# Optimization experiments

Hardware: AMD Instinct MI355X
Metric: run time of the kernel (lower is better)

The kernel has to match this reference:

```python
import jax, jax.numpy as jnp
import numpy as np

N, D, B, C, T, TOD = 8192, 32, 2, 8, 12, 288
PARAM_SCALE = 0.3  # keep relu+softmax logits well-conditioned (original uses plain randn init)


def setup_inputs() -> dict:
    key = jax.random.key(0)
    k0, k1, k2, k3, k4 = jax.random.split(key, 5)
    return {
        "x": jax.random.normal(k0, (B, C, N, T), dtype=jnp.float32),
        "nodevec1": PARAM_SCALE * jax.random.normal(k1, (N, D), dtype=jnp.float32),
        "nodevec2": PARAM_SCALE * jax.random.normal(k2, (N, D), dtype=jnp.float32),
        "timevec": PARAM_SCALE * jax.random.normal(k3, (TOD, D), dtype=jnp.float32),
        "k": PARAM_SCALE * jax.random.normal(k4, (D, D, D), dtype=jnp.float32),
        "time_ind": 100,
    }


def reference(x, nodevec1, nodevec2, timevec, k, time_ind):
    # Dynamic Tucker-decomposition adjacency (SpatialGraphConv.forward, eval mode -> dropout is identity)
    tv = timevec[time_ind]                             # [D]   time_vec
    core = jnp.einsum('d,def->ef', tv, k)              # [D,D] adp1 (squeezed)
    # adp2/adp3 chain: (nodevec1 @ core) @ nodevec2.T  -> [N,N]
    adp = jnp.einsum('ne,ef->nf', nodevec1, core)      # [N,D]
    adp = jnp.einsum('nf,mf->nm', adp, nodevec2)       # [N,N]
    adp = jax.nn.softmax(jax.nn.relu(adp), axis=-1)    # row-softmax over neighbors
    # NConv: neighbor aggregation  'bcnt,nm->bcmt'
    return jnp.einsum('bcnt,nm->bcmt', x, adp)
```

## Files before the change

kernel.cpp:

```cpp
#include <hip/hip_runtime.h>
#include <hip/hip_bf16.h>


#define NN 8192
#define DD 32
#define TT 12
#define NSPLIT 8
#define CHUNK 1024
#define ESTR 72

typedef __attribute__((ext_vector_type(8))) short bf16x8;
typedef __attribute__((ext_vector_type(4))) short bf16x4;
typedef __attribute__((ext_vector_type(4))) float f32x4;

static __device__ __forceinline__ unsigned short f2bf(float f) {
  unsigned int u = __float_as_uint(f);
  u = (u + 0x7FFFu + ((u >> 16) & 1u)) >> 16;
  return (unsigned short)u;
}

__global__ __launch_bounds__(256) void k_prep(const float* __restrict__ nv1,
                                              const float* __restrict__ nv2,
                                              const float* __restrict__ timevec,
                                              const float* __restrict__ kk,
                                              const int* __restrict__ tind,
                                              unsigned short* __restrict__ t1b,
                                              unsigned short* __restrict__ nv2b) {
  __shared__ float cs[1024];
  const int tid = threadIdx.x;
  const float* tv = timevec + (size_t)tind[0] * DD;
  for (int idx = tid; idx < 1024; idx += 256) {
    float acc = 0.f;
#pragma unroll
    for (int d = 0; d < DD; ++d) acc += tv[d] * kk[d * 1024 + idx];
    cs[idx] = acc;
  }
  __syncthreads();
  const int nbase = blockIdx.x * 128;
  const int f = tid & 31, sub = tid >> 5;
#pragma unroll 4
  for (int it = 0; it < 16; ++it) {
    const int n = nbase + it * 8 + sub;
    const float* nr = nv1 + (size_t)n * DD;
    float acc = 0.f;
#pragma unroll
    for (int e = 0; e < DD; ++e) acc += nr[e] * cs[e * DD + f];
    t1b[(size_t)n * DD + f] = f2bf(acc);
  }
#pragma unroll 4
  for (int it = 0; it < 16; ++it) {
    const int idx = nbase * DD + it * 256 + tid;
    nv2b[idx] = f2bf(nv2[idx]);
  }
}

__global__ __launch_bounds__(256) void k_stats(const unsigned short* __restrict__ t1b,
                                               const unsigned short* __restrict__ nv2b,
                                               float* __restrict__ sums) {
  const int tid = threadIdx.x;
  const int w = tid >> 6, lane = tid & 63, q = lane >> 4, i16 = lane & 15;
  const int nbase = blockIdx.x * 64 + w * 16;
  bf16x8 a = *(const bf16x8*)(t1b + (size_t)(nbase + i16) * DD + q * 8);
  const f32x4 z4 = {0.f, 0.f, 0.f, 0.f};
  float s[4] = {0.f, 0.f, 0.f, 0.f};
  const int m0 = blockIdx.y * 2048;
  for (int mt = m0; mt < m0 + 2048; mt += 64) {
#pragma unroll
    for (int u = 0; u < 4; ++u) {
      bf16x8 b = *(const bf16x8*)(nv2b + (size_t)(mt + u * 16 + i16) * DD + q * 8);
      f32x4 d = __builtin_amdgcn_mfma_f32_16x16x32_bf16(a, b, z4, 0, 0, 0);
#pragma unroll
      for (int r = 0; r < 4; ++r) s[r] += __expf(fmaxf(d[r], 0.f));
    }
  }
#pragma unroll
  for (int r = 0; r < 4; ++r)
    for (int off = 1; off < 16; off <<= 1) s[r] += __shfl_xor(s[r], off, 64);
  if (i16 == 0) {
#pragma unroll
    for (int r = 0; r < 4; ++r) atomicAdd(&sums[nbase + q * 4 + r], s[r]);
  }
}

__global__ __launch_bounds__(256) void k_y(const float* __restrict__ x,
                                           const float* __restrict__ sums,
                                           unsigned short* __restrict__ yT) {
  __shared__ float xs[3072];
  const int tid = threadIdx.x;
  const int n0 = blockIdx.x * 256;
  const int bc = blockIdx.y;
  const float* xp = x + (size_t)bc * NN * TT + (size_t)n0 * TT;
#pragma unroll
  for (int j = 0; j < 12; ++j) xs[j * 256 + tid] = xp[j * 256 + tid];
  __syncthreads();
  const float rinv = 1.0f / sums[n0 + tid];
#pragma unroll
  for (int t = 0; t < 12; ++t)
    yT[(size_t)(bc * TT + t) * NN + n0 + tid] = f2bf(xs[tid * 12 + t] * rinv);
}

__global__ __launch_bounds__(256, 2) void k_mega(const unsigned short* __restrict__ t1b,
                                                 const unsigned short* __restrict__ nv2b,
                                                 const unsigned short* __restrict__ yT,
                                                 float* __restrict__ part) {
  const int tid = threadIdx.x;
  const int w = tid >> 6, lane = tid & 63, q = lane >> 4, i16 = lane & 15;
  const int wc = w & 1, wm = w >> 1;
  const int mb = blockIdx.x * 128;
  const int nt0 = blockIdx.y * CHUNK;

  __shared__ unsigned short Ew[2][128][ESTR];

  bf16x8 bg[2];
#pragma unroll
  for (int g = 0; g < 2; ++g)
    bg[g] = *(const bf16x8*)(nv2b + (size_t)(mb + w * 32 + g * 16 + i16) * DD + q * 8);

  const f32x4 z4 = {0.f, 0.f, 0.f, 0.f};
  f32x4 acc[6][4];
#pragma unroll
  for (int c = 0; c < 6; ++c)
#pragma unroll
    for (int ms = 0; ms < 4; ++ms) acc[c][ms] = (f32x4){0.f, 0.f, 0.f, 0.f};

  {
    bf16x8 atL[4];
#pragma unroll
    for (int s = 0; s < 4; ++s)
      atL[s] = *(const bf16x8*)(t1b + (size_t)(nt0 + s * 16 + i16) * DD + q * 8);
#pragma unroll
    for (int g = 0; g < 2; ++g)
#pragma unroll
      for (int s = 0; s < 4; ++s) {
        f32x4 d = __builtin_amdgcn_mfma_f32_16x16x32_bf16(atL[s], bg[g], z4, 0, 0, 0);
        bf16x4 e;
#pragma unroll
        for (int r = 0; r < 4; ++r) e[r] = (short)f2bf(__expf(fmaxf(d[r], 0.f)));
        *(bf16x4*)&Ew[0][w * 32 + g * 16 + i16][s * 16 + q * 4] = e;
      }
  }
  __syncthreads();

  int p = 0;
  for (int st = 0; st < 16; ++st, p ^= 1) {
    const int nt = nt0 + st * 64;
    const bool more = (st < 15);

    bf16x8 atn[4];
    if (more) {
#pragma unroll
      for (int s = 0; s < 4; ++s)
        atn[s] = *(const bf16x8*)(t1b + (size_t)(nt + 64 + s * 16 + i16) * DD + q * 8);
    }

    bf16x8 yfr0[6];
#pragma unroll
    for (int c = 0; c < 6; ++c)
      yfr0[c] = *(const bf16x8*)(yT + (size_t)((wc * 6 + c) * 16 + i16) * NN + nt + q * 8);
    bf16x8 efr0[4];
#pragma unroll
    for (int ms = 0; ms < 4; ++ms)
      efr0[ms] = *(const bf16x8*)&Ew[p][wm * 64 + ms * 16 + i16][q * 8];

    f32x4 d[2][4];
    if (more) {
#pragma unroll
      for (int g = 0; g < 2; ++g)
#pragma unroll
        for (int s = 0; s < 4; ++s)
          d[g][s] = __builtin_amdgcn_mfma_f32_16x16x32_bf16(atn[s], bg[g], z4, 0, 0, 0);
    }

    bf16x8 yfr1[6];
#pragma unroll
    for (int c = 0; c < 6; ++c)
      yfr1[c] = *(const bf16x8*)(yT + (size_t)((wc * 6 + c) * 16 + i16) * NN + nt + 32 + q * 8);
    bf16x8 efr1[4];
#pragma unroll
    for (int ms = 0; ms < 4; ++ms)
      efr1[ms] = *(const bf16x8*)&Ew[p][wm * 64 + ms * 16 + i16][32 + q * 8];

#pragma unroll
    for (int c = 0; c < 6; ++c)
#pragma unroll
      for (int ms = 0; ms < 4; ++ms)
        acc[c][ms] = __builtin_amdgcn_mfma_f32_16x16x32_bf16(yfr0[c], efr0[ms], acc[c][ms], 0, 0, 0);

    if (more) {
#pragma unroll
      for (int g = 0; g < 2; ++g)
#pragma unroll
        for (int s = 0; s < 4; ++s) {
          bf16x4 e;
#pragma unroll
          for (int r = 0; r < 4; ++r) e[r] = (short)f2bf(__expf(fmaxf(d[g][s][r], 0.f)));
          *(bf16x4*)&Ew[p ^ 1][w * 32 + g * 16 + i16][s * 16 + q * 4] = e;
        }
    }

#pragma unroll
    for (int c = 0; c < 6; ++c)
#pragma unroll
      for (int ms = 0; ms < 4; ++ms)
        acc[c][ms] = __builtin_amdgcn_mfma_f32_16x16x32_bf16(yfr1[c], efr1[ms], acc[c][ms], 0, 0, 0);

    __syncthreads();
  }

  float* pp = part + (size_t)blockIdx.y * 192 * NN;
#pragma unroll
  for (int c = 0; c < 6; ++c)
#pragma unroll
    for (int ms = 0; ms < 4; ++ms) {
      const int colbase = (wc * 6 + c) * 16 + q * 4;
      const int m = mb + wm * 64 + ms * 16 + i16;
#pragma unroll
      for (int r = 0; r < 4; ++r)
        pp[(size_t)(colbase + r) * NN + m] = acc[c][ms][r];
    }
}

__global__ __launch_bounds__(256) void k_reduce(const float* __restrict__ part,
                                                float* __restrict__ out) {
  __shared__ float os[3072];
  const int tid = threadIdx.x;
  const int m0 = blockIdx.x * 256;
  const int bc = blockIdx.y;
#pragma unroll
  for (int t = 0; t < 12; ++t) {
    const int col = bc * TT + t;
    float s = 0.f;
#pragma unroll
    for (int nc = 0; nc < NSPLIT; ++nc)
      s += part[((size_t)nc * 192 + col) * NN + m0 + tid];
    os[tid * 12 + t] = s;
  }
  __syncthreads();
  float* op = out + (size_t)bc * NN * TT + (size_t)m0 * TT;
#pragma unroll
  for (int j = 0; j < 12; ++j) op[j * 256 + tid] = os[j * 256 + tid];
}

extern "C" void kernel_launch(void* const* d_in, const int* in_sizes, int n_in,
                              void* d_out, int out_size, void* d_ws, size_t ws_size,
                              hipStream_t stream) {
  const float* x = (const float*)d_in[0];
  const float* nv1 = (const float*)d_in[1];
  const float* nv2 = (const float*)d_in[2];
  const float* tv = (const float*)d_in[3];
  const float* kk = (const float*)d_in[4];
  const int* tind = (const int*)d_in[5];
  float* out = (float*)d_out;

  char* ws = (char*)d_ws;
  unsigned short* t1b  = (unsigned short*)(ws);
  unsigned short* nv2b = (unsigned short*)(ws + 524288);
  float* sums          = (float*)(ws + 1048576);
  unsigned short* yT   = (unsigned short*)(ws + 1081344);
  float* part          = (float*)(ws + 4227072);

  hipMemsetAsync(sums, 0, NN * sizeof(float), stream);
  k_prep<<<64, 256, 0, stream>>>(nv1, nv2, tv, kk, tind, t1b, nv2b);
  k_stats<<<dim3(128, 4), 256, 0, stream>>>(t1b, nv2b, sums);
  k_y<<<dim3(32, 16), 256, 0, stream>>>(x, sums, yT);
  k_mega<<<dim3(64, NSPLIT), 256, 0, stream>>>(t1b, nv2b, yT, part);
  k_reduce<<<dim3(32, 16), 256, 0, stream>>>(part, out);
}
```

Before: 191.4 us.

## Use 8-wave blocks in main kernel, fold log2e into t1b, split stats grid

The main fused kernel moves to 512 threads (8 waves), and each wave now owns half the output columns and one 16-row slice of the exp tile. This cuts per-wave accumulators and registers so more waves can run at once and hide latency better. The log2(e) factor is folded into t1b so exp becomes a raw exp2 instruction, and the stats kernel grid doubles along m to get more parallelism. The cost is more LDS contention per block and more atomics in the stats kernel.

```diff
diff --git a/kernel.cpp b/kernel.cpp
--- a/kernel.cpp
+++ b/kernel.cpp
@@ -17,6 +17,14 @@
   unsigned int u = __float_as_uint(f);
   u = (u + 0x7FFFu + ((u >> 16) & 1u)) >> 16;
   return (unsigned short)u;
+}
+
+static __device__ __forceinline__ float fexp2(float x) {
+#if __has_builtin(__builtin_amdgcn_exp2f)
+  return __builtin_amdgcn_exp2f(x);
+#else
+  return __builtin_exp2f(x);
+#endif
 }
 
 __global__ __launch_bounds__(256) void k_prep(const float* __restrict__ nv1,
@@ -45,7 +53,7 @@
     float acc = 0.f;
 #pragma unroll
     for (int e = 0; e < DD; ++e) acc += nr[e] * cs[e * DD + f];
-    t1b[(size_t)n * DD + f] = f2bf(acc);
+    t1b[(size_t)n * DD + f] = f2bf(acc * 1.4426950408889634f);
   }
 #pragma unroll 4
   for (int it = 0; it < 16; ++it) {
@@ -63,14 +71,14 @@
   bf16x8 a = *(const bf16x8*)(t1b + (size_t)(nbase + i16) * DD + q * 8);
   const f32x4 z4 = {0.f, 0.f, 0.f, 0.f};
   float s[4] = {0.f, 0.f, 0.f, 0.f};
-  const int m0 = blockIdx.y * 2048;
-  for (int mt = m0; mt < m0 + 2048; mt += 64) {
+  const int m0 = blockIdx.y * 1024;
+  for (int mt = m0; mt < m0 + 1024; mt += 64) {
 #pragma unroll
     for (int u = 0; u < 4; ++u) {
       bf16x8 b = *(const bf16x8*)(nv2b + (size_t)(mt + u * 16 + i16) * DD + q * 8);
       f32x4 d = __builtin_amdgcn_mfma_f32_16x16x32_bf16(a, b, z4, 0, 0, 0);
 #pragma unroll
-      for (int r = 0; r < 4; ++r) s[r] += __expf(fmaxf(d[r], 0.f));
+      for (int r = 0; r < 4; ++r) s[r] += fexp2(fmaxf(d[r], 0.f));
     }
   }
 #pragma unroll
@@ -99,45 +107,35 @@
     yT[(size_t)(bc * TT + t) * NN + n0 + tid] = f2bf(xs[tid * 12 + t] * rinv);
 }
 
-__global__ __launch_bounds__(256, 2) void k_mega(const unsigned short* __restrict__ t1b,
+__global__ __launch_bounds__(512, 4) void k_mega(const unsigned short* __restrict__ t1b,
                                                  const unsigned short* __restrict__ nv2b,
                                                  const unsigned short* __restrict__ yT,
                                                  float* __restrict__ part) {
   const int tid = threadIdx.x;
   const int w = tid >> 6, lane = tid & 63, q = lane >> 4, i16 = lane & 15;
-  const int wc = w & 1, wm = w >> 1;
+  const int wc = w >> 1, wm = w & 1;
   const int mb = blockIdx.x * 128;
   const int nt0 = blockIdx.y * CHUNK;
 
   __shared__ unsigned short Ew[2][128][ESTR];
 
-  bf16x8 bg[2];
-#pragma unroll
-  for (int g = 0; g < 2; ++g)
-    bg[g] = *(const bf16x8*)(nv2b + (size_t)(mb + w * 32 + g * 16 + i16) * DD + q * 8);
+  const bf16x8 bg = *(const bf16x8*)(nv2b + (size_t)(mb + w * 16 + i16) * DD + q * 8);
 
   const f32x4 z4 = {0.f, 0.f, 0.f, 0.f};
-  f32x4 acc[6][4];
-#pragma unroll
-  for (int c = 0; c < 6; ++c)
+  f32x4 acc[3][4];
+#pragma unroll
+  for (int c = 0; c < 3; ++c)
 #pragma unroll
     for (int ms = 0; ms < 4; ++ms) acc[c][ms] = (f32x4){0.f, 0.f, 0.f, 0.f};
 
-  {
-    bf16x8 atL[4];
-#pragma unroll
-    for (int s = 0; s < 4; ++s)
-      atL[s] = *(const bf16x8*)(t1b + (size_t)(nt0 + s * 16 + i16) * DD + q * 8);
-#pragma unroll
-    for (int g = 0; g < 2; ++g)
-#pragma unroll
-      for (int s = 0; s < 4; ++s) {
-        f32x4 d = __builtin_amdgcn_mfma_f32_16x16x32_bf16(atL[s], bg[g], z4, 0, 0, 0);
-        bf16x4 e;
-#pragma unroll
-        for (int r = 0; r < 4; ++r) e[r] = (short)f2bf(__expf(fmaxf(d[r], 0.f)));
-        *(bf16x4*)&Ew[0][w * 32 + g * 16 + i16][s * 16 + q * 4] = e;
-      }
+#pragma unroll
+  for (int s = 0; s < 4; ++s) {
+    bf16x8 at = *(const bf16x8*)(t1b + (size_t)(nt0 + s * 16 + i16) * DD + q * 8);
+    f32x4 d = __builtin_amdgcn_mfma_f32_16x16x32_bf16(at, bg, z4, 0, 0, 0);
+    bf16x4 e;
+#pragma unroll
+    for (int r = 0; r < 4; ++r) e[r] = (short)f2bf(fexp2(fmaxf(d[r], 0.f)));
+    *(bf16x4*)&Ew[0][w * 16 + i16][s * 16 + q * 4] = e;
   }
   __syncthreads();
 
@@ -153,66 +151,68 @@
         atn[s] = *(const bf16x8*)(t1b + (size_t)(nt + 64 + s * 16 + i16) * DD + q * 8);
     }
 
-    bf16x8 yfr0[6];
-#pragma unroll
-    for (int c = 0; c < 6; ++c)
-      yfr0[c] = *(const bf16x8*)(yT + (size_t)((wc * 6 + c) * 16 + i16) * NN + nt + q * 8);
-    bf16x8 efr0[4];
+    bf16x8 yfr[3], efr[4];
+#pragma unroll
+    for (int c = 0; c < 3; ++c)
+      yfr[c] = *(const bf16x8*)(yT + (size_t)((wc * 3 + c) * 16 + i16) * NN + nt + q * 8);
 #pragma unroll
     for (int ms = 0; ms < 4; ++ms)
-      efr0[ms] = *(const bf16x8*)&Ew[p][wm * 64 + ms * 16 + i16][q * 8];
-
-    f32x4 d[2][4];
+      efr[ms] = *(const bf16x8*)&Ew[p][wm * 64 + ms * 16 + i16][q * 8];
+
+    f32x4 d0, d1;
     if (more) {
-#pragma unroll
-      for (int g = 0; g < 2; ++g)
-#pragma unroll
-        for (int s = 0; s < 4; ++s)
-          d[g][s] = __builtin_amdgcn_mfma_f32_16x16x32_bf16(atn[s], bg[g], z4, 0, 0, 0);
-    }
-
-    bf16x8 yfr1[6];
-#pragma unroll
-    for (int c = 0; c < 6; ++c)
-      yfr1[c] = *(const bf16x8*)(yT + (size_t)((wc * 6 + c) * 16 + i16) * NN + nt + 32 + q * 8);
-    bf16x8 efr1[4];
+      d0 = __builtin_amdgcn_mfma_f32_16x16x32_bf16(atn[0], bg, z4, 0, 0, 0);
+      d1 = __builtin_amdgcn_mfma_f32_16x16x32_bf16(atn[1], bg, z4, 0, 0, 0);
+    }
+
+#pragma unroll
+    for (int c = 0; c < 3; ++c)
+#pragma unroll
+      for (int ms = 0; ms < 4; ++ms)
+        acc[c][ms] = __builtin_amdgcn_mfma_f32_16x16x32_bf16(yfr[c], efr[ms], acc[c][ms], 0, 0, 0);
+
+    if (more) {
+      bf16x4 e0, e1;
+#pragma unroll
+      for (int r = 0; r < 4; ++r) {
+        e0[r] = (short)f2bf(fexp2(fmaxf(d0[r], 0.f)));
+        e1[r] = (short)f2bf(fexp2(fmaxf(d1[r], 0.f)));
+      }
+      *(bf16x4*)&Ew[p ^ 1][w * 16 + i16][q * 4] = e0;
+      *(bf16x4*)&Ew[p ^ 1][w * 16 + i16][16 + q * 4] = e1;
+      f32x4 d2 = __builtin_amdgcn_mfma_f32_16x16x32_bf16(atn[2], bg, z4, 0, 0, 0);
+      f32x4 d3 = __builtin_amdgcn_mfma_f32_16x16x32_bf16(atn[3], bg, z4, 0, 0, 0);
+      bf16x4 e2, e3;
+#pragma unroll
+      for (int r = 0; r < 4; ++r) {
+        e2[r] = (short)f2bf(fexp2(fmaxf(d2[r], 0.f)));
+        e3[r] = (short)f2bf(fexp2(fmaxf(d3[r], 0.f)));
+      }
+      *(bf16x4*)&Ew[p ^ 1][w * 16 + i16][32 + q * 4] = e2;
+      *(bf16x4*)&Ew[p ^ 1][w * 16 + i16][48 + q * 4] = e3;
+    }
+
+#pragma unroll
+    for (int c = 0; c < 3; ++c)
+      yfr[c] = *(const bf16x8*)(yT + (size_t)((wc * 3 + c) * 16 + i16) * NN + nt + 32 + q * 8);
 #pragma unroll
     for (int ms = 0; ms < 4; ++ms)
-      efr1[ms] = *(const bf16x8*)&Ew[p][wm * 64 + ms * 16 + i16][32 + q * 8];
-
-#pragma unroll
-    for (int c = 0; c < 6; ++c)
+      efr[ms] = *(const bf16x8*)&Ew[p][wm * 64 + ms * 16 + i16][32 + q * 8];
+#pragma unroll
+    for (int c = 0; c < 3; ++c)
 #pragma unroll
       for (int ms = 0; ms < 4; ++ms)
-        acc[c][ms] = __builtin_amdgcn_mfma_f32_16x16x32_bf16(yfr0[c], efr0[ms], acc[c][ms], 0, 0, 0);
-
-    if (more) {
-#pragma unroll
-      for (int g = 0; g < 2; ++g)
-#pragma unroll
-        for (int s = 0; s < 4; ++s) {
-          bf16x4 e;
-#pragma unroll
-          for (int r = 0; r < 4; ++r) e[r] = (short)f2bf(__expf(fmaxf(d[g][s][r], 0.f)));
-          *(bf16x4*)&Ew[p ^ 1][w * 32 + g * 16 + i16][s * 16 + q * 4] = e;
-        }
-    }
-
-#pragma unroll
-    for (int c = 0; c < 6; ++c)
-#pragma unroll
-      for (int ms = 0; ms < 4; ++ms)
-        acc[c][ms] = __builtin_amdgcn_mfma_f32_16x16x32_bf16(yfr1[c], efr1[ms], acc[c][ms], 0, 0, 0);
+        acc[c][ms] = __builtin_amdgcn_mfma_f32_16x16x32_bf16(yfr[c], efr[ms], acc[c][ms], 0, 0, 0);
 
     __syncthreads();
   }
 
   float* pp = part + (size_t)blockIdx.y * 192 * NN;
 #pragma unroll
-  for (int c = 0; c < 6; ++c)
+  for (int c = 0; c < 3; ++c)
 #pragma unroll
     for (int ms = 0; ms < 4; ++ms) {
-      const int colbase = (wc * 6 + c) * 16 + q * 4;
+      const int colbase = (wc * 3 + c) * 16 + q * 4;
       const int m = mb + wm * 64 + ms * 16 + i16;
 #pragma unroll
       for (int r = 0; r < 4; ++r)
@@ -261,8 +261,8 @@
 
   hipMemsetAsync(sums, 0, NN * sizeof(float), stream);
   k_prep<<<64, 256, 0, stream>>>(nv1, nv2, tv, kk, tind, t1b, nv2b);
-  k_stats<<<dim3(128, 4), 256, 0, stream>>>(t1b, nv2b, sums);
+  k_stats<<<dim3(128, 8), 256, 0, stream>>>(t1b, nv2b, sums);
   k_y<<<dim3(32, 16), 256, 0, stream>>>(x, sums, yT);
-  k_mega<<<dim3(64, NSPLIT), 256, 0, stream>>>(t1b, nv2b, yT, part);
+  k_mega<<<dim3(64, NSPLIT), 512, 0, stream>>>(t1b, nv2b, yT, part);
   k_reduce<<<dim3(32, 16), 256, 0, stream>>>(part, out);
 }
```

New measurement: 180.8 us. -5.6%, faster.
